# Performance work log

Measured on AMD Instinct MI355X. Metric: run time of the kernel, lower is better.

## Reference

```python
import jax, jax.numpy as jnp
import numpy as np

B, S, D, H, E = 2, 2048, 1024, 2048, 8


def setup_inputs() -> dict:
    key = jax.random.key(0)
    ks = jax.random.split(key, 5)
    scale_in = 0.02
    x = jax.random.normal(ks[0], (B, S, D), dtype=jnp.float32)
    Wr = jax.random.normal(ks[1], (D, E), dtype=jnp.float32) * scale_in
    br = jnp.zeros((E,), dtype=jnp.float32)
    W1 = jax.random.normal(ks[2], (E, D, H), dtype=jnp.float32) * (1.0 / np.sqrt(D))
    b1 = jnp.zeros((E, H), dtype=jnp.float32)
    W2 = jax.random.normal(ks[3], (E, H, D), dtype=jnp.float32) * (1.0 / np.sqrt(H))
    b2 = jnp.zeros((E, D), dtype=jnp.float32)
    return {"x": x, "Wr": Wr, "br": br, "W1": W1, "b1": b1, "W2": W2, "b2": b2, "k": 2}


def reference(x, Wr, br, W1, b1, W2, b2, k):
    # Router: top-k logits, softmax over the k selected logits
    logits = x @ Wr + br                       # [B,S,E]
    top_v, top_i = jax.lax.top_k(logits, k)    # [B,S,k]
    scores = jax.nn.softmax(top_v, axis=-1)    # [B,S,k]

    # Dense all-expert MLP (reference combine): [B,S,E,*]
    h = jax.nn.relu(jnp.einsum('bsd,edh->bseh', x, W1) + b1[None, None])
    eo = jnp.einsum('bseh,ehd->bsed', h, W2) + b2[None, None]  # [B,S,E,D]

    # Gather the k selected experts per token and combine with scores
    sel = jnp.take_along_axis(eo, top_i[..., None], axis=2)   # [B,S,k,D]
    out = jnp.sum(scores[..., None] * sel, axis=2)             # [B,S,D]
    return out
```

## Files before the change

kernel.cpp:

```cpp
#include <hip/hip_runtime.h>
#include <hip/hip_bf16.h>

#define TOKENS 4096
#define DDIM 1024
#define HDIM 2048
#define NEXP 8
#define NASSIGN 8192
#define MAX_TILES 80

typedef __attribute__((ext_vector_type(8))) __bf16 bf16x8;
typedef __attribute__((ext_vector_type(4))) float f32x4;
typedef __attribute__((ext_vector_type(4))) unsigned short u16x4;

__device__ __forceinline__ unsigned short f2bf(float f) {
    unsigned int u = __builtin_bit_cast(unsigned int, f);
    u += 0x7fffu + ((u >> 16) & 1u);
    return (unsigned short)(u >> 16);
}

__global__ __launch_bounds__(256) void router_kernel(
    const float* __restrict__ x, const float* __restrict__ Wr, const float* __restrict__ br,
    unsigned short* __restrict__ x_bf, int* __restrict__ topk_e, float* __restrict__ topk_s)
{
    const int t = blockIdx.x * 4 + (threadIdx.x >> 6);
    const int lane = threadIdx.x & 63;
    const float* xr = x + (long)t * DDIM;
    unsigned short* xo = x_bf + (long)t * DDIM;
    float acc[8] = {0.f,0.f,0.f,0.f,0.f,0.f,0.f,0.f};
    for (int it = 0; it < DDIM / 64; ++it) {
        const int d = it * 64 + lane;
        const float xv = xr[d];
        xo[d] = f2bf(xv);
        const float4 w0 = *(const float4*)(Wr + d * 8);
        const float4 w1 = *(const float4*)(Wr + d * 8 + 4);
        acc[0] += xv * w0.x; acc[1] += xv * w0.y; acc[2] += xv * w0.z; acc[3] += xv * w0.w;
        acc[4] += xv * w1.x; acc[5] += xv * w1.y; acc[6] += xv * w1.z; acc[7] += xv * w1.w;
    }
#pragma unroll
    for (int e = 0; e < 8; ++e) {
        float v = acc[e];
        for (int off = 32; off > 0; off >>= 1) v += __shfl_down(v, off, 64);
        acc[e] = v;
    }
    if (lane == 0) {
        float lg[8];
#pragma unroll
        for (int e = 0; e < 8; ++e) lg[e] = acc[e] + br[e];
        int i0 = 0; float v0 = lg[0];
#pragma unroll
        for (int e = 1; e < 8; ++e) if (lg[e] > v0) { v0 = lg[e]; i0 = e; }
        int i1 = -1; float v1 = -3.4e38f;
#pragma unroll
        for (int e = 0; e < 8; ++e) if (e != i0 && lg[e] > v1) { v1 = lg[e]; i1 = e; }
        const float e1 = expf(v1 - v0);
        const float inv = 1.f / (1.f + e1);
        topk_e[t * 2]     = i0; topk_s[t * 2]     = inv;
        topk_e[t * 2 + 1] = i1; topk_s[t * 2 + 1] = e1 * inv;
    }
}

__global__ __launch_bounds__(1024) void build_lists_kernel(
    const int* __restrict__ topk_e, const float* __restrict__ topk_s,
    int* __restrict__ token_list, float* __restrict__ score_list, int* __restrict__ meta)
{
    __shared__ int cnt[NEXP];
    __shared__ int base[NEXP];
    __shared__ int cur[NEXP];
    const int tid = threadIdx.x;
    if (tid < NEXP) cnt[tid] = 0;
    __syncthreads();
    for (int i = tid; i < NASSIGN; i += 1024) atomicAdd(&cnt[topk_e[i]], 1);
    __syncthreads();
    if (tid == 0) {
        int accu = 0;
        for (int e = 0; e < NEXP; ++e) { base[e] = accu; cur[e] = accu; accu += cnt[e]; }
        int ntile = 0;
        for (int e = 0; e < NEXP; ++e) {
            const int c = cnt[e];
            for (int r = 0; r * 128 < c; ++r) {
                meta[1 + ntile] = e;
                meta[1 + MAX_TILES + ntile] = base[e] + r * 128;
                meta[1 + 2 * MAX_TILES + ntile] = (c - r * 128) < 128 ? (c - r * 128) : 128;
                ++ntile;
            }
        }
        meta[0] = ntile;
    }
    __syncthreads();
    for (int i = tid; i < NASSIGN; i += 1024) {
        const int e = topk_e[i];
        const int slot = atomicAdd(&cur[e], 1);
        token_list[slot] = i >> 1;
        score_list[slot] = topk_s[i];
    }
}

__global__ __launch_bounds__(256) void transpose_cvt_kernel(
    const float* __restrict__ W1, const float* __restrict__ W2,
    unsigned short* __restrict__ W1t, unsigned short* __restrict__ W2t)
{
    __shared__ unsigned short tile[64 * 68];
    const int z = blockIdx.y;
    const bool is1 = z < 8;
    const int e = is1 ? z : z - 8;
    const int K = is1 ? DDIM : HDIM;
    const int N = is1 ? HDIM : DDIM;
    const float* src = (is1 ? W1 : W2) + (long)e * K * N;
    unsigned short* dst = (is1 ? W1t : W2t) + (long)e * K * N;
    const int ktiles = K >> 6;
    const int k0 = (blockIdx.x % ktiles) * 64;
    const int n0 = (blockIdx.x / ktiles) * 64;
    const int r0 = threadIdx.x >> 4;
    const int c4 = (threadIdx.x & 15) * 4;
#pragma unroll
    for (int i = 0; i < 4; ++i) {
        const int r = r0 + i * 16;
        const float4 v = *(const float4*)(src + (long)(k0 + r) * N + n0 + c4);
        tile[(c4 + 0) * 68 + r] = f2bf(v.x);
        tile[(c4 + 1) * 68 + r] = f2bf(v.y);
        tile[(c4 + 2) * 68 + r] = f2bf(v.z);
        tile[(c4 + 3) * 68 + r] = f2bf(v.w);
    }
    __syncthreads();
#pragma unroll
    for (int i = 0; i < 4; ++i) {
        const int rn = r0 + i * 16;
        u16x4 o;
        o.x = tile[rn * 68 + c4 + 0];
        o.y = tile[rn * 68 + c4 + 1];
        o.z = tile[rn * 68 + c4 + 2];
        o.w = tile[rn * 68 + c4 + 3];
        *(u16x4*)(dst + (long)(n0 + rn) * K + k0 + c4) = o;
    }
}

template<int KDIM, int NDIM, bool G2>
__global__ __launch_bounds__(256, 2) void expert_gemm(
    const unsigned short* __restrict__ Abase,
    const unsigned short* __restrict__ Bt,
    const float* __restrict__ bias,
    unsigned short* __restrict__ Hout,
    float* __restrict__ Out,
    const int* __restrict__ token_list,
    const float* __restrict__ score_list,
    const int* __restrict__ meta)
{
    const int nt = meta[0];
    const int xcd = blockIdx.x & 7;
    const int off = blockIdx.x >> 3;
    const int q = nt >> 3;
    const int r = nt & 7;
    const int cnt_i = q + (xcd < r ? 1 : 0);
    if (off >= cnt_i) return;
    const int t = xcd * q + (xcd < r ? xcd : r) + off;
    const int e = meta[1 + t];
    const int slot0 = meta[1 + MAX_TILES + t];
    const int rows_valid = meta[1 + 2 * MAX_TILES + t];
    const int n0 = blockIdx.y * 128;

    __shared__ unsigned short As[2][128 * 32];
    __shared__ unsigned short Bs[2][128 * 32];

    const int tid = threadIdx.x;
    const int lane = tid & 63;
    const int w = tid >> 6;
    const int wm = w & 1;
    const int wn = w >> 1;
    const int quad = lane >> 4;
    const int l15 = lane & 15;

    const unsigned short* aptr[2];
    const unsigned short* bptr[2];
    int ldsoff[2];
#pragma unroll
    for (int c = 0; c < 2; ++c) {
        const int chunk = c * 256 + tid;
        const int row = chunk >> 2;
        const int kc = (chunk & 3) ^ ((row >> 1) & 3);
        const int rr = row < rows_valid ? row : rows_valid - 1;
        const long arow = G2 ? (long)(slot0 + rr) : (long)token_list[slot0 + rr];
        aptr[c] = Abase + arow * (long)KDIM + kc * 8;
        bptr[c] = Bt + ((long)e * NDIM + n0 + row) * (long)KDIM + kc * 8;
        ldsoff[c] = (c * 256 + w * 64) * 8;
    }

    f32x4 acc[4][4] = {};
    constexpr int NITER = KDIM / 32;

    auto issue = [&](int buf, int kof) {
#pragma unroll
        for (int c = 0; c < 2; ++c)
            __builtin_amdgcn_global_load_lds(
                (const __attribute__((address_space(1))) unsigned int*)(aptr[c] + kof),
                (__attribute__((address_space(3))) unsigned int*)&As[buf][ldsoff[c]], 16, 0, 0);
#pragma unroll
        for (int c = 0; c < 2; ++c)
            __builtin_amdgcn_global_load_lds(
                (const __attribute__((address_space(1))) unsigned int*)(bptr[c] + kof),
                (__attribute__((address_space(3))) unsigned int*)&Bs[buf][ldsoff[c]], 16, 0, 0);
    };

    auto compute = [&](int buf) {
        const unsigned short* Ab = As[buf];
        const unsigned short* Bb = Bs[buf];
        const int slot = (quad ^ ((l15 >> 1) & 3)) * 8;
        bf16x8 af[4], bfr[4];
#pragma unroll
        for (int mi = 0; mi < 4; ++mi)
            af[mi] = *(const bf16x8*)&Ab[(wm * 64 + mi * 16 + l15) * 32 + slot];
#pragma unroll
        for (int ni = 0; ni < 4; ++ni)
            bfr[ni] = *(const bf16x8*)&Bb[(wn * 64 + ni * 16 + l15) * 32 + slot];
#pragma unroll
        for (int mi = 0; mi < 4; ++mi)
#pragma unroll
            for (int ni = 0; ni < 4; ++ni)
                acc[mi][ni] = __builtin_amdgcn_mfma_f32_16x16x32_bf16(af[mi], bfr[ni], acc[mi][ni], 0, 0, 0);
    };

    issue(0, 0);
#pragma unroll 1
    for (int k = 0; k < NITER - 1; ++k) {
        issue((k + 1) & 1, (k + 1) * 32);
        asm volatile("s_waitcnt vmcnt(4)\n\ts_barrier" ::: "memory");
        compute(k & 1);
        asm volatile("s_barrier" ::: "memory");
    }
    asm volatile("s_waitcnt vmcnt(0)\n\ts_barrier" ::: "memory");
    compute((NITER - 1) & 1);

#pragma unroll
    for (int mi = 0; mi < 4; ++mi) {
#pragma unroll
        for (int ni = 0; ni < 4; ++ni) {
            const int col = n0 + wn * 64 + ni * 16 + l15;
#pragma unroll
            for (int rr = 0; rr < 4; ++rr) {
                const int row = wm * 64 + mi * 16 + quad * 4 + rr;
                if (row < rows_valid) {
                    float v = acc[mi][ni][rr] + bias[e * NDIM + col];
                    if (!G2) {
                        v = v > 0.f ? v : 0.f;
                        Hout[(long)(slot0 + row) * NDIM + col] = f2bf(v);
                    } else {
                        const int slot = slot0 + row;
                        const int tok = token_list[slot];
                        const float s = score_list[slot];
                        unsafeAtomicAdd(&Out[(long)tok * NDIM + col], s * v);
                    }
                }
            }
        }
    }
}

extern "C" void kernel_launch(void* const* d_in, const int* in_sizes, int n_in,
                              void* d_out, int out_size, void* d_ws, size_t ws_size,
                              hipStream_t stream)
{
    (void)in_sizes; (void)n_in; (void)out_size; (void)ws_size;
    const float* x  = (const float*)d_in[0];
    const float* Wr = (const float*)d_in[1];
    const float* br = (const float*)d_in[2];
    const float* W1 = (const float*)d_in[3];
    const float* b1 = (const float*)d_in[4];
    const float* W2 = (const float*)d_in[5];
    const float* b2 = (const float*)d_in[6];
    float* out = (float*)d_out;

    char* ws = (char*)d_ws;
    unsigned short* x_bf  = (unsigned short*)(ws);
    unsigned short* W1t   = (unsigned short*)(ws + 8388608);
    unsigned short* W2t   = (unsigned short*)(ws + 41943040);
    unsigned short* hbuf  = (unsigned short*)(ws + 75497472);
    int*   topk_e     = (int*)(ws + 109051904);
    float* topk_s     = (float*)(ws + 109084672);
    int*   token_list = (int*)(ws + 109117440);
    float* score_list = (float*)(ws + 109150208);
    int*   meta       = (int*)(ws + 109182976);

    hipMemsetAsync(d_out, 0, (size_t)TOKENS * DDIM * sizeof(float), stream);

    router_kernel<<<TOKENS / 4, 256, 0, stream>>>(x, Wr, br, x_bf, topk_e, topk_s);
    build_lists_kernel<<<1, 1024, 0, stream>>>(topk_e, topk_s, token_list, score_list, meta);
    transpose_cvt_kernel<<<dim3(512, 16), 256, 0, stream>>>(W1, W2, W1t, W2t);
    expert_gemm<DDIM, HDIM, false><<<dim3(MAX_TILES, HDIM / 128), 256, 0, stream>>>(
        x_bf, W1t, b1, hbuf, nullptr, token_list, score_list, meta);
    expert_gemm<HDIM, DDIM, true><<<dim3(MAX_TILES, DDIM / 128), 256, 0, stream>>>(
        hbuf, W2t, b2, nullptr, out, token_list, score_list, meta);
}
```

Before: 353.3 us.

## Triple-buffer expert GEMM loads, fold output zeroing into router, ballot-based list build

The expert GEMM moves from a two-stage to a three-stage LDS ring, so loads are issued two K-steps ahead, and occupancy is hinted at 3 blocks per CU. The separate memset of the output is replaced by zeroing inside the router kernel, which saves one launch. The list-building kernel uses wavefront ballots and popcounts in place of per-element shared atomics. Together these aim to hide global load latency and cut launch and atomic overhead, but the deeper ring raises LDS use and may limit occupancy. The vmcnt(4) wait is unchanged even though two stages are now in flight, which may let compute read a buffer that is not yet loaded.

```diff
diff --git a/kernel.cpp b/kernel.cpp
--- a/kernel.cpp
+++ b/kernel.cpp
@@ -20,8 +20,14 @@
 
 __global__ __launch_bounds__(256) void router_kernel(
     const float* __restrict__ x, const float* __restrict__ Wr, const float* __restrict__ br,
-    unsigned short* __restrict__ x_bf, int* __restrict__ topk_e, float* __restrict__ topk_s)
-{
+    unsigned short* __restrict__ x_bf, int* __restrict__ topk_e, float* __restrict__ topk_s,
+    float* __restrict__ out)
+{
+    {
+        float4* o4 = (float4*)(out + (long)blockIdx.x * 4 * DDIM);
+        const float4 z = {0.f, 0.f, 0.f, 0.f};
+        for (int i = threadIdx.x; i < DDIM; i += 256) o4[i] = z;
+    }
     const int t = blockIdx.x * 4 + (threadIdx.x >> 6);
     const int lane = threadIdx.x & 63;
     const float* xr = x + (long)t * DDIM;
@@ -64,34 +70,58 @@
     int* __restrict__ token_list, float* __restrict__ score_list, int* __restrict__ meta)
 {
     __shared__ int cnt[NEXP];
-    __shared__ int base[NEXP];
     __shared__ int cur[NEXP];
     const int tid = threadIdx.x;
+    const int lane = tid & 63;
     if (tid < NEXP) cnt[tid] = 0;
     __syncthreads();
-    for (int i = tid; i < NASSIGN; i += 1024) atomicAdd(&cnt[topk_e[i]], 1);
+    {
+        int acc = 0;
+        for (int it = 0; it < NASSIGN / 1024; ++it) {
+            const int e = topk_e[it * 1024 + tid];
+#pragma unroll
+            for (int ee = 0; ee < NEXP; ++ee) {
+                const unsigned long long m = __ballot(e == ee);
+                if (lane == ee) acc += __popcll(m);
+            }
+        }
+        if (lane < NEXP) atomicAdd(&cnt[lane], acc);
+    }
     __syncthreads();
     if (tid == 0) {
-        int accu = 0;
-        for (int e = 0; e < NEXP; ++e) { base[e] = accu; cur[e] = accu; accu += cnt[e]; }
-        int ntile = 0;
+        int accu = 0, ntile = 0;
         for (int e = 0; e < NEXP; ++e) {
             const int c = cnt[e];
+            cur[e] = accu;
             for (int r = 0; r * 128 < c; ++r) {
                 meta[1 + ntile] = e;
-                meta[1 + MAX_TILES + ntile] = base[e] + r * 128;
+                meta[1 + MAX_TILES + ntile] = accu + r * 128;
                 meta[1 + 2 * MAX_TILES + ntile] = (c - r * 128) < 128 ? (c - r * 128) : 128;
                 ++ntile;
             }
+            accu += c;
         }
         meta[0] = ntile;
     }
     __syncthreads();
-    for (int i = tid; i < NASSIGN; i += 1024) {
-        const int e = topk_e[i];
-        const int slot = atomicAdd(&cur[e], 1);
-        token_list[slot] = i >> 1;
-        score_list[slot] = topk_s[i];
+    for (int it = 0; it < NASSIGN / 1024; ++it) {
+        const int idx = it * 1024 + tid;
+        const int e = topk_e[idx];
+        const float s = topk_s[idx];
+        int pos = 0;
+#pragma unroll
+        for (int ee = 0; ee < NEXP; ++ee) {
+            const unsigned long long m = __ballot(e == ee);
+            if (e == ee) {
+                const int leader = __ffsll((long long)m) - 1;
+                int wbase = 0;
+                if (lane == leader) wbase = atomicAdd(&cur[ee], __popcll(m));
+                wbase = __shfl(wbase, leader, 64);
+                pos = wbase + __popcll(m & ((1ull << lane) - 1ull));
+            }
+        }
+        token_list[pos] = idx >> 1;
+        score_list[pos] = s;
     }
 }
 
@@ -135,7 +165,7 @@
 }
 
 template<int KDIM, int NDIM, bool G2>
-__global__ __launch_bounds__(256, 2) void expert_gemm(
+__global__ __launch_bounds__(256, 3) void expert_gemm(
     const unsigned short* __restrict__ Abase,
     const unsigned short* __restrict__ Bt,
     const float* __restrict__ bias,
@@ -158,8 +188,8 @@
     const int rows_valid = meta[1 + 2 * MAX_TILES + t];
     const int n0 = blockIdx.y * 128;
 
-    __shared__ unsigned short As[2][128 * 32];
-    __shared__ unsigned short Bs[2][128 * 32];
+    __shared__ unsigned short As[3][128 * 32];
+    __shared__ unsigned short Bs[3][128 * 32];
 
     const int tid = threadIdx.x;
     const int lane = tid & 63;
@@ -187,7 +217,8 @@
     f32x4 acc[4][4] = {};
     constexpr int NITER = KDIM / 32;
 
-    auto issue = [&](int buf, int kof) {
+    auto issue = [&](int buf, int k) {
+        const int kof = k * 32;
 #pragma unroll
         for (int c = 0; c < 2; ++c)
             __builtin_amdgcn_global_load_lds(
@@ -219,15 +250,16 @@
     };
 
     issue(0, 0);
+    issue(1, 1);
 #pragma unroll 1
     for (int k = 0; k < NITER - 1; ++k) {
-        issue((k + 1) & 1, (k + 1) * 32);
         asm volatile("s_waitcnt vmcnt(4)\n\ts_barrier" ::: "memory");
-        compute(k & 1);
+        compute(k % 3);
         asm volatile("s_barrier" ::: "memory");
+        if (k + 2 < NITER) issue((k + 2) % 3, k + 2);
     }
     asm volatile("s_waitcnt vmcnt(0)\n\ts_barrier" ::: "memory");
-    compute((NITER - 1) & 1);
+    compute((NITER - 1) % 3);
 
 #pragma unroll
     for (int mi = 0; mi < 4; ++mi) {
@@ -279,9 +311,7 @@
     float* score_list = (float*)(ws + 109150208);
     int*   meta       = (int*)(ws + 109182976);
 
-    hipMemsetAsync(d_out, 0, (size_t)TOKENS * DDIM * sizeof(float), stream);
-
-    router_kernel<<<TOKENS / 4, 256, 0, stream>>>(x, Wr, br, x_bf, topk_e, topk_s);
+    router_kernel<<<TOKENS / 4, 256, 0, stream>>>(x, Wr, br, x_bf, topk_e, topk_s, out);
     build_lists_kernel<<<1, 1024, 0, stream>>>(topk_e, topk_s, token_list, score_list, meta);
     transpose_cvt_kernel<<<dim3(512, 16), 256, 0, stream>>>(W1, W2, W1t, W2t);
     expert_gemm<DDIM, HDIM, false><<<dim3(MAX_TILES, HDIM / 128), 256, 0, stream>>>(
```

Measured after the change: 356.2 us. Within noise of the previous version (+0.8%).
